# Kernel tuning notes

Measured on AMD Instinct MI355X. Metric: run time of the kernel, lower is better.

## Reference

```python
import jax, jax.numpy as jnp
import numpy as np

N, E, NFEAT, NHID = 50000, 800000, 256, 128
EPS = 1e-5


def setup_inputs() -> dict:
    key = jax.random.key(0)
    ks = jax.random.split(key, 12)
    s = 0.05
    return {
        "x": jax.random.normal(ks[0], (N, NFEAT), jnp.float32),
        "adj": jax.random.randint(ks[1], (2, E), 0, N, jnp.int32),
        "features": jax.random.uniform(ks[2], (E,), jnp.float32),
        "W_in": jax.random.normal(ks[3], (NHID, NFEAT), jnp.float32) * s,
        "b_in": jnp.zeros((NHID,), jnp.float32),
        "W1_rel": jax.random.normal(ks[4], (NHID, NHID), jnp.float32) * s,
        "b1_rel": jnp.zeros((NHID,), jnp.float32),
        "W1_root": jax.random.normal(ks[5], (NHID, NHID), jnp.float32) * s,
        "W2_rel": jax.random.normal(ks[6], (NHID, NHID), jnp.float32) * s,
        "b2_rel": jnp.zeros((NHID,), jnp.float32),
        "W2_root": jax.random.normal(ks[7], (NHID, NHID), jnp.float32) * s,
        "gamma": jnp.ones((NHID,), jnp.float32),
        "beta": jnp.zeros((NHID,), jnp.float32),
    }


def _graph_conv(h, src, dst, ew, W_rel, b_rel, W_root):
    # torch_geometric GraphConv (aggr='add'):
    #   out_i = W_rel @ (sum_{j->i} e_ji * h_j) + b_rel + W_root @ h_i
    msg = h[src] * ew[:, None]                       # [E, NHID] gather
    agg = jax.ops.segment_sum(msg, dst, num_segments=N)  # [N, NHID] scatter-add
    return agg @ W_rel.T + b_rel + h @ W_root.T


def _batch_norm(h, gamma, beta):
    mu = h.mean(axis=0)
    var = h.var(axis=0)
    return (h - mu) * jax.lax.rsqrt(var + EPS) * gamma + beta


def reference(x, adj, features, W_in, b_in, W1_rel, b1_rel, W1_root,
              W2_rel, b2_rel, W2_root, gamma, beta):
    src, dst = adj[0], adj[1]
    h = jax.nn.relu(x @ W_in.T + b_in)               # linear_in + relu (dropout=identity in eval)
    h = _graph_conv(h, src, dst, features, W1_rel, b1_rel, W1_root)
    h = jax.nn.relu(_batch_norm(h, gamma, beta))     # batch1 + relu
    h = _graph_conv(h, src, dst, features, W2_rel, b2_rel, W2_root)
    return _batch_norm(h, gamma, beta)               # batch1 reused (per source)
```

## Files before the change

kernel.cpp:

```cpp
#include <hip/hip_runtime.h>
#include <hip/hip_bf16.h>

#define NNODES 50000
#define NEDGES 800000
#define NF 256
#define NH 128
#define BN_EPS 1e-5f
#define MTILES (NNODES / 16)
#define GEMM_BLOCKS 1024
#define CONV_BLOCKS 391
#define NBUCKETS 196
#define BCAP 4608
#define SCAT_BLOCKS ((NEDGES + 2047) / 2048)
#define WC2_BLOCKS 256
#define FRONT_BLOCKS (SCAT_BLOCKS + WC2_BLOCKS + GEMM_BLOCKS)

typedef __attribute__((ext_vector_type(8))) __bf16 bf16x8;
typedef __attribute__((ext_vector_type(4))) float floatx4;

__device__ __forceinline__ __hip_bfloat16 f2bf(float f) { return __float2bfloat16(f); }
__device__ __forceinline__ float bits2f(unsigned short b) {
    union { unsigned u; float f; } u; u.u = ((unsigned)b) << 16; return u.f;
}

__device__ __forceinline__ bf16x8 cvt8(const float* __restrict__ p) {
    floatx4 a0 = *(const floatx4*)p;
    floatx4 a1 = *(const floatx4*)(p + 4);
    bf16x8 r;
    r[0] = (__bf16)a0[0]; r[1] = (__bf16)a0[1]; r[2] = (__bf16)a0[2]; r[3] = (__bf16)a0[3];
    r[4] = (__bf16)a1[0]; r[5] = (__bf16)a1[1]; r[6] = (__bf16)a1[2]; r[7] = (__bf16)a1[3];
    return r;
}

__global__ __launch_bounds__(256, 2) void front_kernel(
    const int* __restrict__ adj, const float* __restrict__ ew,
    int* __restrict__ gcursor, uint2* __restrict__ pairbuf,
    unsigned char* __restrict__ nodebuf,
    const float* __restrict__ W1r, const float* __restrict__ W1o,
    const float* __restrict__ W2r, const float* __restrict__ W2o,
    __hip_bfloat16* __restrict__ wbf,
    const float* __restrict__ X, const float* __restrict__ W_in,
    const float* __restrict__ b_in, __hip_bfloat16* __restrict__ h0)
{
    __shared__ int cnt[NBUCKETS];
    __shared__ int base[NBUCKETS];
    const int tid = threadIdx.x;
    const int bid = blockIdx.x;

    if (bid >= SCAT_BLOCKS + WC2_BLOCKS) {
        const int waveG = (bid - SCAT_BLOCKS - WC2_BLOCKS) * 4 + (tid >> 6);
        const int lane = tid & 63;
        const int half = waveG & 1;
        const int ar = lane & 15;
        const int q  = lane >> 4;

        bf16x8 bw[4][8];
        float bv[4];
        #pragma unroll
        for (int t = 0; t < 4; ++t) {
            const int row = half * 64 + t * 16 + ar;
            bv[t] = b_in[row];
            #pragma unroll
            for (int k = 0; k < 8; ++k)
                bw[t][k] = cvt8(W_in + (size_t)row * NF + k * 32 + q * 8);
        }

        for (int strip = waveG >> 1; strip < MTILES; strip += GEMM_BLOCKS * 2) {
            const int m0 = strip << 4;
            floatx4 acc[4] = {};
            #pragma unroll
            for (int k = 0; k < 8; ++k) {
                const bf16x8 a = cvt8(X + (size_t)(m0 + ar) * NF + k * 32 + q * 8);
                #pragma unroll
                for (int t = 0; t < 4; ++t)
                    acc[t] = __builtin_amdgcn_mfma_f32_16x16x32_bf16(a, bw[t][k], acc[t], 0, 0, 0);
            }
            #pragma unroll
            for (int t = 0; t < 4; ++t) {
                const int col = half * 64 + t * 16 + ar;
                #pragma unroll
                for (int r = 0; r < 4; ++r) {
                    const float v = fmaxf(acc[t][r] + bv[t], 0.f);
                    h0[(size_t)(m0 + q * 4 + r) * NH + col] = f2bf(v);
                }
            }
        }
        return;
    }

    if (bid >= SCAT_BLOCKS) {
        const int i = (bid - SCAT_BLOCKS) * 256 + tid;
        const float* src; int off;
        if (i < 16384)      { src = W1r; off = i; }
        else if (i < 32768) { src = W1o; off = i - 16384; }
        else if (i < 49152) { src = W2r; off = i - 32768; }
        else                { src = W2o; off = i - 49152; }
        wbf[i] = f2bf(src[off]);
        return;
    }

    if (tid < NBUCKETS) cnt[tid] = 0;
    __syncthreads();
    const int e0 = bid * 2048;
    #pragma unroll
    for (int i = 0; i < 8; ++i) {
        const int e = e0 + i * 256 + tid;
        if (e < NEDGES) atomicAdd(&cnt[adj[NEDGES + e] >> 8], 1);
    }
    __syncthreads();
    if (tid < NBUCKETS) {
        base[tid] = tid * BCAP + atomicAdd(&gcursor[tid], cnt[tid]);
        cnt[tid] = 0;
    }
    __syncthreads();
    #pragma unroll
    for (int i = 0; i < 8; ++i) {
        const int e = e0 + i * 256 + tid;
        if (e >= NEDGES) continue;
        const int dst = adj[NEDGES + e];
        const int b = dst >> 8;
        const int off = atomicAdd(&cnt[b], 1);
        const int slot = base[b] + off;
        if (slot < (b + 1) * BCAP) {
            pairbuf[slot] = make_uint2((unsigned)adj[e], __float_as_uint(ew[e]));
            nodebuf[slot] = (unsigned char)(dst & 255);
        }
    }
}

__global__ __launch_bounds__(256) void bucket_sort_kernel(
    const int* __restrict__ gcursor, const uint2* __restrict__ pairbuf,
    const unsigned char* __restrict__ nodebuf, uint2* __restrict__ sorted,
    int* __restrict__ rowptr, int* __restrict__ rowend)
{
    const int b = blockIdx.x;
    const int tid = threadIdx.x;
    const int capbase = b * BCAP;
    int n = gcursor[b];
    if (n > BCAP) n = BCAP;

    __shared__ int cnt[256];
    __shared__ int s[256];
    cnt[tid] = 0;
    __syncthreads();
    for (int j = tid; j < n; j += 256)
        atomicAdd(&cnt[nodebuf[capbase + j]], 1);
    __syncthreads();
    const int v = cnt[tid];
    s[tid] = v;
    __syncthreads();
    for (int off = 1; off < 256; off <<= 1) {
        const int t = (tid >= off) ? s[tid - off] : 0;
        __syncthreads();
        s[tid] += t;
        __syncthreads();
    }
    const int excl = s[tid] - v;
    const int node = b * 256 + tid;
    if (node < NNODES) {
        rowptr[node] = capbase + excl;
        rowend[node] = capbase + excl + v;
    }
    cnt[tid] = excl;
    __syncthreads();
    for (int j = tid; j < n; j += 256) {
        const int nd = nodebuf[capbase + j];
        const int pos = atomicAdd(&cnt[nd], 1);
        sorted[capbase + pos] = pairbuf[capbase + j];
    }
}

__global__ __launch_bounds__(256) void gather_kernel(
    const uint2* __restrict__ sorted, const int* __restrict__ rowptr,
    const int* __restrict__ rowend,
    const __hip_bfloat16* __restrict__ h, __hip_bfloat16* __restrict__ agg)
{
    const int node = blockIdx.x * 4 + (threadIdx.x >> 6);
    if (node >= NNODES) return;
    const int lane = threadIdx.x & 63;
    const int beg = rowptr[node];
    const int end = rowend[node];
    const unsigned short* hb = (const unsigned short*)h;

    float a0[8] = {}, a1[8] = {};

    int j = beg;
    if ((j & 1) && j < end) {
        const uint2 ev = sorted[j++];
        const float w = __uint_as_float(ev.y);
        const unsigned raw = *(const unsigned*)(hb + (size_t)ev.x * NH + lane * 2);
        a0[0] += w * bits2f((unsigned short)(raw & 0xffffu));
        a1[0] += w * bits2f((unsigned short)(raw >> 16));
    }
    for (; j + 8 <= end; j += 8) {
        const uint4 e01 = *(const uint4*)(sorted + j);
        const uint4 e23 = *(const uint4*)(sorted + j + 2);
        const uint4 e45 = *(const uint4*)(sorted + j + 4);
        const uint4 e67 = *(const uint4*)(sorted + j + 6);
        const unsigned r0 = *(const unsigned*)(hb + (size_t)e01.x * NH + lane * 2);
        const unsigned r1 = *(const unsigned*)(hb + (size_t)e01.z * NH + lane * 2);
        const unsigned r2 = *(const unsigned*)(hb + (size_t)e23.x * NH + lane * 2);
        const unsigned r3 = *(const unsigned*)(hb + (size_t)e23.z * NH + lane * 2);
        const unsigned r4 = *(const unsigned*)(hb + (size_t)e45.x * NH + lane * 2);
        const unsigned r5 = *(const unsigned*)(hb + (size_t)e45.z * NH + lane * 2);
        const unsigned r6 = *(const unsigned*)(hb + (size_t)e67.x * NH + lane * 2);
        const unsigned r7 = *(const unsigned*)(hb + (size_t)e67.z * NH + lane * 2);
        const float w0 = __uint_as_float(e01.y), w1 = __uint_as_float(e01.w);
        const float w2 = __uint_as_float(e23.y), w3 = __uint_as_float(e23.w);
        const float w4 = __uint_as_float(e45.y), w5 = __uint_as_float(e45.w);
        const float w6 = __uint_as_float(e67.y), w7 = __uint_as_float(e67.w);
        a0[0] += w0 * bits2f((unsigned short)(r0 & 0xffffu));
        a1[0] += w0 * bits2f((unsigned short)(r0 >> 16));
        a0[1] += w1 * bits2f((unsigned short)(r1 & 0xffffu));
        a1[1] += w1 * bits2f((unsigned short)(r1 >> 16));
        a0[2] += w2 * bits2f((unsigned short)(r2 & 0xffffu));
        a1[2] += w2 * bits2f((unsigned short)(r2 >> 16));
        a0[3] += w3 * bits2f((unsigned short)(r3 & 0xffffu));
        a1[3] += w3 * bits2f((unsigned short)(r3 >> 16));
        a0[4] += w4 * bits2f((unsigned short)(r4 & 0xffffu));
        a1[4] += w4 * bits2f((unsigned short)(r4 >> 16));
        a0[5] += w5 * bits2f((unsigned short)(r5 & 0xffffu));
        a1[5] += w5 * bits2f((unsigned short)(r5 >> 16));
        a0[6] += w6 * bits2f((unsigned short)(r6 & 0xffffu));
        a1[6] += w6 * bits2f((unsigned short)(r6 >> 16));
        a0[7] += w7 * bits2f((unsigned short)(r7 & 0xffffu));
        a1[7] += w7 * bits2f((unsigned short)(r7 >> 16));
    }
    for (; j + 2 <= end; j += 2) {
        const uint4 e01 = *(const uint4*)(sorted + j);
        const unsigned r0 = *(const unsigned*)(hb + (size_t)e01.x * NH + lane * 2);
        const unsigned r1 = *(const unsigned*)(hb + (size_t)e01.z * NH + lane * 2);
        const float w0 = __uint_as_float(e01.y), w1 = __uint_as_float(e01.w);
        a0[0] += w0 * bits2f((unsigned short)(r0 & 0xffffu));
        a1[0] += w0 * bits2f((unsigned short)(r0 >> 16));
        a0[1] += w1 * bits2f((unsigned short)(r1 & 0xffffu));
        a1[1] += w1 * bits2f((unsigned short)(r1 >> 16));
    }
    if (j < end) {
        const uint2 ev = sorted[j];
        const float w = __uint_as_float(ev.y);
        const unsigned raw = *(const unsigned*)(hb + (size_t)ev.x * NH + lane * 2);
        a0[0] += w * bits2f((unsigned short)(raw & 0xffffu));
        a1[0] += w * bits2f((unsigned short)(raw >> 16));
    }
    const float f0 = ((a0[0] + a0[1]) + (a0[2] + a0[3])) + ((a0[4] + a0[5]) + (a0[6] + a0[7]));
    const float f1 = ((a1[0] + a1[1]) + (a1[2] + a1[3])) + ((a1[4] + a1[5]) + (a1[6] + a1[7]));
    unsigned o = ((unsigned)__bfloat16_as_ushort(f2bf(f1)) << 16) |
                 (unsigned)__bfloat16_as_ushort(f2bf(f0));
    *(unsigned*)((unsigned short*)agg + (size_t)node * NH + lane * 2) = o;
}

__global__ __launch_bounds__(512, 4) void gemm_conv_kernel(
    const __hip_bfloat16* __restrict__ agg, const __hip_bfloat16* __restrict__ h,
    const __hip_bfloat16* __restrict__ Wrel, const __hip_bfloat16* __restrict__ Wroot,
    const float* __restrict__ bias, float* __restrict__ out,
    float* __restrict__ stats)
{
    __shared__ char wlds[65536];
    __shared__ float sst[256];
    const int tid = threadIdx.x;
    if (tid < 256) sst[tid] = 0.f;

    {
        const int r = tid >> 2, part = tid & 3;
        const int mat = part >> 1;
        const int t8 = r >> 4, ar8 = r & 15;
        const __hip_bfloat16* wsrc =
            (mat ? Wroot : Wrel) + (size_t)r * NH + (part & 1) * 64;
        #pragma unroll
        for (int j = 0; j < 8; ++j) {
            const int col0 = (part & 1) * 64 + j * 8;
            const int kk = col0 >> 5, qq = (col0 >> 3) & 3;
            const int F = ((mat * 8 + t8) * 4 + kk) * 4 + qq;
            *(bf16x8*)(wlds + F * 256 + ar8 * 16) = *(const bf16x8*)(wsrc + j * 8);
        }
    }
    __syncthreads();

    const int wv = tid >> 6, lane = tid & 63;
    const int ar = lane & 15, q = lane >> 4;
    const int strip = blockIdx.x * 8 + wv;

    if (strip < MTILES) {
        const int m0 = strip << 4;
        const char* wl = wlds + q * 256 + ar * 16;

        floatx4 acc[8] = {};
        #pragma unroll
        for (int kk = 0; kk < 4; ++kk) {
            const bf16x8 a = *(const bf16x8*)(agg + (size_t)(m0 + ar) * NH + kk * 32 + q * 8);
            #pragma unroll
            for (int t = 0; t < 8; ++t)
                acc[t] = __builtin_amdgcn_mfma_f32_16x16x32_bf16(
                    a, *(const bf16x8*)(wl + ((t * 4 + kk) * 4) * 256), acc[t], 0, 0, 0);
        }
        #pragma unroll
        for (int kk = 0; kk < 4; ++kk) {
            const bf16x8 a = *(const bf16x8*)(h + (size_t)(m0 + ar) * NH + kk * 32 + q * 8);
            #pragma unroll
            for (int t = 0; t < 8; ++t)
                acc[t] = __builtin_amdgcn_mfma_f32_16x16x32_bf16(
                    a, *(const bf16x8*)(wl + (((8 + t) * 4 + kk) * 4) * 256), acc[t], 0, 0, 0);
        }

        #pragma unroll
        for (int t = 0; t < 8; ++t) {
            const float bvt = bias[t * 16 + ar];
            float s1 = 0.f, s2 = 0.f;
            #pragma unroll
            for (int r2 = 0; r2 < 4; ++r2) {
                const float v = acc[t][r2] + bvt;
                out[(size_t)(m0 + q * 4 + r2) * NH + t * 16 + ar] = v;
                s1 += v; s2 += v * v;
            }
            s1 += __shfl_xor(s1, 16, 64); s1 += __shfl_xor(s1, 32, 64);
            s2 += __shfl_xor(s2, 16, 64); s2 += __shfl_xor(s2, 32, 64);
            if (q == 0) {
                atomicAdd(&sst[t * 16 + ar], s1);
                atomicAdd(&sst[128 + t * 16 + ar], s2);
            }
        }
    }
    __syncthreads();
    if (tid < 256) unsafeAtomicAdd(&stats[tid], sst[tid]);
}

__global__ __launch_bounds__(256) void bn_relu_bf16_kernel(
    const float* __restrict__ t, const float* __restrict__ stats,
    const float* __restrict__ gamma, const float* __restrict__ beta,
    __hip_bfloat16* __restrict__ out)
{
    const size_t i = ((size_t)blockIdx.x * 256 + threadIdx.x) * 4;
    const float inv_n = 1.0f / (float)NNODES;
    const floatx4 v = *(const floatx4*)(t + i);
    ushort4 o;
    unsigned short* op = (unsigned short*)&o;
    #pragma unroll
    for (int j = 0; j < 4; ++j) {
        const int c = (int)((i + j) & (NH - 1));
        const float mu = stats[c] * inv_n;
        const float var = stats[128 + c] * inv_n - mu * mu;
        const float rs = rsqrtf(var + BN_EPS);
        const float y = (v[j] - mu) * rs * gamma[c] + beta[c];
        op[j] = __bfloat16_as_ushort(f2bf(fmaxf(y, 0.f)));
    }
    *(ushort4*)((unsigned short*)out + i) = o;
}

__global__ __launch_bounds__(256) void bn_f32_kernel(
    const float* __restrict__ t, const float* __restrict__ stats,
    const float* __restrict__ gamma, const float* __restrict__ beta,
    float* __restrict__ out)
{
    const size_t i = ((size_t)blockIdx.x * 256 + threadIdx.x) * 4;
    const float inv_n = 1.0f / (float)NNODES;
    const floatx4 v = *(const floatx4*)(t + i);
    floatx4 o;
    #pragma unroll
    for (int j = 0; j < 4; ++j) {
        const int c = (int)((i + j) & (NH - 1));
        const float mu = stats[c] * inv_n;
        const float var = stats[128 + c] * inv_n - mu * mu;
        const float rs = rsqrtf(var + BN_EPS);
        o[j] = (v[j] - mu) * rs * gamma[c] + beta[c];
    }
    *(floatx4*)(out + i) = o;
}


extern "C" void kernel_launch(void* const* d_in, const int* in_sizes, int n_in,
                              void* d_out, int out_size, void* d_ws, size_t ws_size,
                              hipStream_t stream)
{
    const float* x    = (const float*)d_in[0];
    const int*   adj  = (const int*)d_in[1];
    const float* ew   = (const float*)d_in[2];
    const float* W_in = (const float*)d_in[3];
    const float* b_in = (const float*)d_in[4];
    const float* W1r  = (const float*)d_in[5];
    const float* b1   = (const float*)d_in[6];
    const float* W1o  = (const float*)d_in[7];
    const float* W2r  = (const float*)d_in[8];
    const float* b2   = (const float*)d_in[9];
    const float* W2o  = (const float*)d_in[10];
    const float* gmm  = (const float*)d_in[11];
    const float* bta  = (const float*)d_in[12];
    float* out = (float*)d_out;
    float* t   = (float*)d_out;

    char* ws = (char*)d_ws;
    __hip_bfloat16* h0  = (__hip_bfloat16*)ws; ws += (size_t)NNODES * NH * 2;
    __hip_bfloat16* h1  = (__hip_bfloat16*)ws; ws += (size_t)NNODES * NH * 2;
    __hip_bfloat16* agg = (__hip_bfloat16*)ws; ws += (size_t)NNODES * NH * 2;
    uint2*          sorted  = (uint2*)ws;      ws += (size_t)NBUCKETS * BCAP * 8;
    uint2*          pairbuf = (uint2*)ws;      ws += (size_t)NBUCKETS * BCAP * 8;
    unsigned char*  nodebuf = (unsigned char*)ws; ws += (size_t)NBUCKETS * BCAP;
    int*            rowptr  = (int*)ws;        ws += NNODES * 4;
    int*            rowend  = (int*)ws;        ws += NNODES * 4;
    int*            gcursor = (int*)ws;        ws += 256 * 4;
    float*          st1     = (float*)ws;      ws += 256 * 4;
    float*          st2     = (float*)ws;      ws += 256 * 4;
    __hip_bfloat16* wbf     = (__hip_bfloat16*)ws; ws += 65536 * 2;

    const __hip_bfloat16* Wb1r = wbf;
    const __hip_bfloat16* Wb1o = wbf + 16384;
    const __hip_bfloat16* Wb2r = wbf + 32768;
    const __hip_bfloat16* Wb2o = wbf + 49152;

    const int node_blocks = (NNODES + 3) / 4;
    const int bn_blocks   = (NNODES * NH) / (256 * 4);

    hipMemsetAsync(gcursor, 0, 3 * 256 * 4, stream);
    front_kernel<<<FRONT_BLOCKS, 256, 0, stream>>>(
        adj, ew, gcursor, pairbuf, nodebuf, W1r, W1o, W2r, W2o, wbf,
        x, W_in, b_in, h0);
    bucket_sort_kernel<<<NBUCKETS, 256, 0, stream>>>(gcursor, pairbuf, nodebuf,
                                                     sorted, rowptr, rowend);

    gather_kernel<<<node_blocks, 256, 0, stream>>>(sorted, rowptr, rowend, h0, agg);
    gemm_conv_kernel<<<CONV_BLOCKS, 512, 0, stream>>>(agg, h0, Wb1r, Wb1o, b1, t, st1);
    bn_relu_bf16_kernel<<<bn_blocks, 256, 0, stream>>>(t, st1, gmm, bta, h1);

    gather_kernel<<<node_blocks, 256, 0, stream>>>(sorted, rowptr, rowend, h1, agg);
    gemm_conv_kernel<<<CONV_BLOCKS, 512, 0, stream>>>(agg, h1, Wb2r, Wb2o, b2, t, st2);
    bn_f32_kernel<<<bn_blocks, 256, 0, stream>>>(t, st2, gmm, bta, out);
}
```

Measured before the change: 311.7 us.

## Stage W_in in shared memory and compute full 128-column strips per wave

The input-projection GEMM in the front kernel now converts W_in to bf16 once per block into a 64 KB shared-memory buffer laid out in MFMA fragment order. Previously each wave held half of W_in in registers and two waves redundantly re-read each X strip. Now each wave computes all 128 output columns for one 16-row strip, so every X row is loaded once. Blocks grow to 512 threads and the scatter and weight-convert roles are re-indexed to match. The 64 KB LDS allocation also applies to the scatter blocks, which may limit how many blocks fit on a CU at once.

Measured after the change: 284.2 us. 1.1x faster.

```diff
diff --git a/kernel.cpp b/kernel.cpp
--- a/kernel.cpp
+++ b/kernel.cpp
@@ -7,13 +7,13 @@
 #define NH 128
 #define BN_EPS 1e-5f
 #define MTILES (NNODES / 16)
-#define GEMM_BLOCKS 1024
 #define CONV_BLOCKS 391
 #define NBUCKETS 196
 #define BCAP 4608
-#define SCAT_BLOCKS ((NEDGES + 2047) / 2048)
-#define WC2_BLOCKS 256
-#define FRONT_BLOCKS (SCAT_BLOCKS + WC2_BLOCKS + GEMM_BLOCKS)
+#define GEMM_BLOCKS 391
+#define SCAT_BLOCKS 391
+#define WC2_BLOCKS 128
+#define FRONT_BLOCKS (GEMM_BLOCKS + SCAT_BLOCKS + WC2_BLOCKS)
 
 typedef __attribute__((ext_vector_type(8))) __bf16 bf16x8;
 typedef __attribute__((ext_vector_type(4))) float floatx4;
@@ -32,7 +32,7 @@
     return r;
 }
 
-__global__ __launch_bounds__(256, 2) void front_kernel(
+__global__ __launch_bounds__(512, 4) void front_kernel(
     const int* __restrict__ adj, const float* __restrict__ ew,
     int* __restrict__ gcursor, uint2* __restrict__ pairbuf,
     unsigned char* __restrict__ nodebuf,
@@ -42,54 +42,56 @@
     const float* __restrict__ X, const float* __restrict__ W_in,
     const float* __restrict__ b_in, __hip_bfloat16* __restrict__ h0)
 {
-    __shared__ int cnt[NBUCKETS];
-    __shared__ int base[NBUCKETS];
+    __shared__ char smem[65536];
     const int tid = threadIdx.x;
     const int bid = blockIdx.x;
 
-    if (bid >= SCAT_BLOCKS + WC2_BLOCKS) {
-        const int waveG = (bid - SCAT_BLOCKS - WC2_BLOCKS) * 4 + (tid >> 6);
-        const int lane = tid & 63;
-        const int half = waveG & 1;
-        const int ar = lane & 15;
-        const int q  = lane >> 4;
-
-        bf16x8 bw[4][8];
-        float bv[4];
-        #pragma unroll
-        for (int t = 0; t < 4; ++t) {
-            const int row = half * 64 + t * 16 + ar;
-            bv[t] = b_in[row];
-            #pragma unroll
-            for (int k = 0; k < 8; ++k)
-                bw[t][k] = cvt8(W_in + (size_t)row * NF + k * 32 + q * 8);
-        }
-
-        for (int strip = waveG >> 1; strip < MTILES; strip += GEMM_BLOCKS * 2) {
+    if (bid < GEMM_BLOCKS) {
+        {
+            const int r = tid >> 2, part = tid & 3;
+            const int t8 = r >> 4, ar8 = r & 15;
+            const float* wsrc = W_in + (size_t)r * NF + part * 64;
+            #pragma unroll
+            for (int j = 0; j < 8; ++j) {
+                const int col0 = part * 64 + j * 8;
+                const int kk = col0 >> 5, qq = (col0 >> 3) & 3;
+                const int F = (t8 * 8 + kk) * 4 + qq;
+                *(bf16x8*)(smem + F * 256 + ar8 * 16) = cvt8(wsrc + j * 8);
+            }
+        }
+        __syncthreads();
+
+        const int wv = tid >> 6, lane = tid & 63;
+        const int ar = lane & 15, q = lane >> 4;
+        const int strip = bid * 8 + wv;
+        if (strip < MTILES) {
             const int m0 = strip << 4;
-            floatx4 acc[4] = {};
-            #pragma unroll
-            for (int k = 0; k < 8; ++k) {
-                const bf16x8 a = cvt8(X + (size_t)(m0 + ar) * NF + k * 32 + q * 8);
+            const char* wl = smem + q * 256 + ar * 16;
+
+            floatx4 acc[8] = {};
+            #pragma unroll
+            for (int kk = 0; kk < 8; ++kk) {
+                const bf16x8 a = cvt8(X + (size_t)(m0 + ar) * NF + kk * 32 + q * 8);
                 #pragma unroll
-                for (int t = 0; t < 4; ++t)
-                    acc[t] = __builtin_amdgcn_mfma_f32_16x16x32_bf16(a, bw[t][k], acc[t], 0, 0, 0);
+                for (int t = 0; t < 8; ++t)
+                    acc[t] = __builtin_amdgcn_mfma_f32_16x16x32_bf16(
+                        a, *(const bf16x8*)(wl + ((t * 8 + kk) * 4) * 256), acc[t], 0, 0, 0);
             }
             #pragma unroll
-            for (int t = 0; t < 4; ++t) {
-                const int col = half * 64 + t * 16 + ar;
+            for (int t = 0; t < 8; ++t) {
+                const float bvt = b_in[t * 16 + ar];
                 #pragma unroll
-                for (int r = 0; r < 4; ++r) {
-                    const float v = fmaxf(acc[t][r] + bv[t], 0.f);
-                    h0[(size_t)(m0 + q * 4 + r) * NH + col] = f2bf(v);
+                for (int r2 = 0; r2 < 4; ++r2) {
+                    const float v = fmaxf(acc[t][r2] + bvt, 0.f);
+                    h0[(size_t)(m0 + q * 4 + r2) * NH + t * 16 + ar] = f2bf(v);
                 }
             }
         }
         return;
     }
 
-    if (bid >= SCAT_BLOCKS) {
-        const int i = (bid - SCAT_BLOCKS) * 256 + tid;
+    if (bid >= GEMM_BLOCKS + SCAT_BLOCKS) {
+        const int i = (bid - GEMM_BLOCKS - SCAT_BLOCKS) * 512 + tid;
         const float* src; int off;
         if (i < 16384)      { src = W1r; off = i; }
         else if (i < 32768) { src = W1o; off = i - 16384; }
@@ -99,12 +101,14 @@
         return;
     }
 
+    int* cnt  = (int*)smem;
+    int* base = (int*)(smem + 1024);
     if (tid < NBUCKETS) cnt[tid] = 0;
     __syncthreads();
-    const int e0 = bid * 2048;
+    const int e0 = (bid - GEMM_BLOCKS) * 2048;
     #pragma unroll
-    for (int i = 0; i < 8; ++i) {
-        const int e = e0 + i * 256 + tid;
+    for (int i = 0; i < 4; ++i) {
+        const int e = e0 + i * 512 + tid;
         if (e < NEDGES) atomicAdd(&cnt[adj[NEDGES + e] >> 8], 1);
     }
     __syncthreads();
@@ -114,8 +118,8 @@
     }
     __syncthreads();
     #pragma unroll
-    for (int i = 0; i < 8; ++i) {
-        const int e = e0 + i * 256 + tid;
+    for (int i = 0; i < 4; ++i) {
+        const int e = e0 + i * 512 + tid;
         if (e >= NEDGES) continue;
         const int dst = adj[NEDGES + e];
         const int b = dst >> 8;
@@ -411,7 +415,7 @@
     const int bn_blocks   = (NNODES * NH) / (256 * 4);
 
     hipMemsetAsync(gcursor, 0, 3 * 256 * 4, stream);
-    front_kernel<<<FRONT_BLOCKS, 256, 0, stream>>>(
+    front_kernel<<<FRONT_BLOCKS, 512, 0, stream>>>(
         adj, ew, gcursor, pairbuf, nodebuf, W1r, W1o, W2r, W2o, wbf,
         x, W_in, b_in, h0);
     bucket_sort_kernel<<<NBUCKETS, 256, 0, stream>>>(gcursor, pairbuf, nodebuf,
```
